# Kernel tuning notes

Hardware: AMD Instinct MI355X
Metric: run time of the kernel (lower is better)

## Reference

```python
import jax, jax.numpy as jnp
import numpy as np

DROP_PROB = 0.1
BLOCK_SIZE = 7  # odd -> no even-size trim branch
N, C, H, W = 64, 256, 28, 28


def conv3x3(x, w):
    # x: [N,C,H,W], w: [O,I,3,3], stride 1, SAME padding
    return jax.lax.conv_general_dilated(
        x, w, window_strides=(1, 1), padding='SAME',
        dimension_numbers=('NCHW', 'OIHW', 'NCHW'))


def setup_inputs() -> dict:
    key = jax.random.key(0)
    k1, k2, k3, k4 = jax.random.split(key, 4)
    x = jax.random.normal(k1, (N, C, H, W), jnp.float32)
    # learned conv weights for the two branches (layer3 and premodel.layer3)
    w_layer3 = jax.random.normal(k2, (C, C, 3, 3), jnp.float32) * 0.05
    w_pre = jax.random.normal(k3, (C, C, 3, 3), jnp.float32) * 0.05
    # uniform draws used for the Bernoulli(gamma) drop mask, shape (N,H,W)
    mask_u = jax.random.uniform(k4, (N, H, W), jnp.float32)
    return {'x': x, 'w_layer3': w_layer3, 'w_pre': w_pre, 'mask_u': mask_u}


def reference(x, w_layer3, w_pre, mask_u):
    gamma = DROP_PROB / (BLOCK_SIZE ** 2)
    a = conv3x3(x, w_layer3)   # x = self.layer3(x)
    b = conv3x3(x, w_pre)      # output4 = self.premodel.layer3(x)
    # mask = (rand(N,H,W) < gamma).float()
    mask = (mask_u < gamma).astype(x.dtype)  # [N,H,W]
    # block_mask = 1 - max_pool2d(mask, k=block_size, stride=1, pad=block_size//2)
    pooled = jax.lax.reduce_window(
        mask, -jnp.inf, jax.lax.max,
        window_dimensions=(1, BLOCK_SIZE, BLOCK_SIZE),
        window_strides=(1, 1, 1), padding='SAME')
    block_mask = 1.0 - pooled  # [N,H,W]
    # fused blend: keep layer3 output where block_mask==1, else premodel output
    out = jnp.where(block_mask[:, None, :, :] == 1.0, a, b)  # [N,C,H,W]
    # out * block_mask.numel() / block_mask.sum()
    scale = jnp.asarray(block_mask.size, x.dtype) / jnp.sum(block_mask)
    return out * scale
```

## Files before the change

### kernel.cpp

```cpp
#include <hip/hip_runtime.h>
#include <hip/hip_bf16.h>


typedef __bf16  bf16x8 __attribute__((ext_vector_type(8)));
typedef float   f32x4  __attribute__((ext_vector_type(4)));
typedef short   short8 __attribute__((ext_vector_type(8)));
typedef unsigned int u32;
typedef unsigned short u16;

#define XT_OFF     65536
#define WT_OFF     29556736
#define LISTA_OFF  31916032
#define LISTB_OFF  32116736
#define SLOT       22528

__device__ __forceinline__ u16 f2bf(float v) {
    u32 u = __float_as_uint(v);
    u32 r = (u + 0x7FFFu + ((u >> 16) & 1u)) >> 16;
    return (u16)r;
}

__device__ __forceinline__ void gll16(const void* g, void* l) {
    __builtin_amdgcn_global_load_lds(
        (const __attribute__((address_space(1))) u32*)g,
        (__attribute__((address_space(3))) u32*)l, 16, 0, 0);
}

__global__ void prep_kernel(const float* __restrict__ x,
                            const float* __restrict__ wl,
                            const float* __restrict__ wp,
                            const float* __restrict__ mu,
                            u16* __restrict__ xt, u16* __restrict__ wt,
                            int* __restrict__ listA, int* __restrict__ listB,
                            int* __restrict__ cntB, int* __restrict__ cntA) {
    int b = blockIdx.x, tid = threadIdx.x;
    if (b < 1920) {
        int n = b / 30, oh = b % 30;
        u16* row = xt + (size_t)(n * 30 + oh) * 30 * 256;
        if (oh == 0 || oh == 29) {
            u32* r32 = (u32*)row;
            #pragma unroll
            for (int i = 0; i < 15; ++i) r32[i * 256 + tid] = 0;
            return;
        }
        int h = oh - 1;
        row[tid] = 0;
        row[29 * 256 + tid] = 0;
        const float* src = x + ((size_t)(n * 256 + tid) * 28 + h) * 28;
        float f[28];
        #pragma unroll
        for (int q = 0; q < 7; ++q) {
            float4 v = *(const float4*)(src + q * 4);
            f[q * 4 + 0] = v.x; f[q * 4 + 1] = v.y;
            f[q * 4 + 2] = v.z; f[q * 4 + 3] = v.w;
        }
        #pragma unroll
        for (int w = 0; w < 28; ++w)
            row[(1 + w) * 256 + tid] = f2bf(f[w]);
    } else if (b < 2496) {
        int gid = (b - 1920) * 256 + tid;
        int base = gid << 3;
        int bb = base >> 12;
        int e = base & 4095;
        int t = bb >> 2, nq = bb & 3;
        int kk = t >> 3;
        int row = e >> 5, ps = (e & 31) >> 3;
        int c0 = (t & 7) * 32 + ((ps ^ ((row >> 1) & 3)) << 3);
        int o = nq * 128 + row;
        const float* wsrc = (o < 256) ? wl : wp;
        const float* wr = wsrc + ((size_t)(o & 255) * 256 + c0) * 9 + kk;
        short8 v;
        #pragma unroll
        for (int j = 0; j < 8; ++j) v[j] = (short)f2bf(wr[j * 9]);
        *(short8*)(wt + base) = v;
    } else {
        __shared__ int wbase[8];
        int m = (b - 2496) * 256 + tid;
        int n = m / 784, rem = m % 784;
        int h = rem / 28, w = rem % 28;
        const float g = (float)(0.1 / 49.0);
        const float* un = mu + n * 784;
        int p = 0;
        for (int dy = -3; dy <= 3; ++dy) {
            int hh = h + dy;
            if (hh < 0 || hh >= 28) continue;
            for (int dx = -3; dx <= 3; ++dx) {
                int ww = w + dx;
                if (ww < 0 || ww >= 28) continue;
                p |= (un[hh * 28 + ww] < g) ? 1 : 0;
            }
        }
        unsigned long long ball = __ballot(p);
        int wid = tid >> 6, ln = tid & 63;
        int c1 = __popcll(ball);
        if (ln == 0) {
            wbase[wid]     = atomicAdd(cntB, c1);
            wbase[4 + wid] = atomicAdd(cntA, 64 - c1);
        }
        __syncthreads();
        int rank1 = __popcll(ball & ((1ULL << ln) - 1));
        int rank0 = ln - rank1;
        if (p) listB[wbase[wid] + rank1] = m;
        else   listA[wbase[4 + wid] + rank0] = m;
    }
}

__global__ __launch_bounds__(256, 2)
void conv_kernel(const char* __restrict__ xt,
                 const char* __restrict__ wt,
                 const int* __restrict__ listA,
                 const int* __restrict__ listB,
                 const int* __restrict__ dropped,
                 float* __restrict__ out) {
    __shared__ char smem[55296];
    const int tid = threadIdx.x;
    const int lb = (blockIdx.x & 7) * 57 + (blockIdx.x >> 3);
    const int vt = lb >> 1;
    const int nh = lb & 1;
    const int cB = *dropped;
    const int cA = 50176 - cB;
    const int naT = (cA + 223) / 224;
    const int nbT = (cB + 223) / 224;
    if (vt >= naT + nbT) return;
    const int branch = (vt >= naT) ? 1 : 0;
    const int tix = branch ? (vt - naT) : vt;
    const int cnt = branch ? cB : cA;
    const int* lst = branch ? listB : listA;
    const int nq = branch * 2 + nh;
    const int lane = tid & 63, wave = tid >> 6;
    const int lane15 = lane & 15, grp = lane >> 4;
    const int wm = wave >> 1, wn = wave & 1;

    long pbA[4];
    {
        int swz = ((tid & 3) ^ ((tid >> 3) & 3)) << 4;
        #pragma unroll
        for (int i = 0; i < 4; ++i) {
            int r = i * 64 + (tid >> 2);
            int idx = tix * 224 + r;
            if (idx >= cnt) idx = cnt - 1;
            int m = lst[idx];
            int n = m / 784, rem = m % 784;
            pbA[i] = (long)(((n * 30 + rem / 28 + 1) * 30 + (rem % 28 + 1)) * 512
                            + swz);
        }
    }

    f32x4 acc[7][4];
    #pragma unroll
    for (int i = 0; i < 7; ++i)
        #pragma unroll
        for (int j = 0; j < 4; ++j)
            acc[i][j] = (f32x4){0.f, 0.f, 0.f, 0.f};

    const int so  = (grp ^ ((lane15 >> 1) & 3)) << 4;
    const int arb = wm * 7168 + (lane15 << 6) + so;
    const int brb = 14336 + wn * 4096 + (lane15 << 6) + so;

#define AON(TC) ((long)((TC) >> 3) / 3 * 15360 + (long)(((TC) >> 3) % 3) * 512 \
                 - 15872 + (long)(((TC) & 7) << 6))
#define STG(TC, SL) { char* sd_ = smem + (SL) * SLOT;                       \
        const long ao_ = AON(TC);                                           \
        gll16(xt + pbA[0] + ao_, sd_ + (tid << 4));                         \
        gll16(xt + pbA[1] + ao_, sd_ + 4096 + (tid << 4));                  \
        gll16(xt + pbA[2] + ao_, sd_ + 8192 + (tid << 4));                  \
        if (tid < 128) gll16(xt + pbA[3] + ao_, sd_ + 12288 + (tid << 4));  \
        const char* wb_ = wt + ((size_t)((TC) * 4 + nq) << 13);             \
        gll16(wb_ + (tid << 4), sd_ + 14336 + (tid << 4));                  \
        gll16(wb_ + 4096 + (tid << 4), sd_ + 18432 + (tid << 4)); }
#define DS_AV0(dst, SL) { const char* sb_ = smem + (SL) * SLOT;             \
        _Pragma("unroll")                                                   \
        for (int fm = 0; fm < 4; ++fm)                                      \
            dst[fm] = *(const bf16x8*)(sb_ + arb + (fm << 10)); }
#define DS_AV1(dst, SL) { const char* sb_ = smem + (SL) * SLOT + 4096;      \
        _Pragma("unroll")                                                   \
        for (int fm = 0; fm < 3; ++fm)                                      \
            dst[fm] = *(const bf16x8*)(sb_ + arb + (fm << 10)); }
#define DS_BV(dst, SL) { const char* sb_ = smem + (SL) * SLOT;              \
        _Pragma("unroll")                                                   \
        for (int fn = 0; fn < 4; ++fn)                                      \
            dst[fn] = *(const bf16x8*)(sb_ + brb + (fn << 10)); }
#define MM(A0_, NF, AV, BV) { __builtin_amdgcn_s_setprio(1);                \
        _Pragma("unroll")                                                   \
        for (int fm = 0; fm < (NF); ++fm)                                   \
            _Pragma("unroll")                                               \
            for (int fn = 0; fn < 4; ++fn)                                  \
                acc[(A0_)+fm][fn] = __builtin_amdgcn_mfma_f32_16x16x32_bf16( \
                    AV[fm], BV[fn], acc[(A0_)+fm][fn], 0, 0, 0);            \
        __builtin_amdgcn_s_setprio(0); }
#define LGKM(N) { asm volatile("s_waitcnt lgkmcnt(" #N ")" ::: "memory");   \
                  __builtin_amdgcn_sched_barrier(0); }
#define VM0     { asm volatile("s_waitcnt vmcnt(0)" ::: "memory");          \
                  __builtin_amdgcn_sched_barrier(0); }
#define BAR     asm volatile("s_barrier" ::: "memory")

    bf16x8 av0[4], av1[3], bv[4];

    STG(0, 0);
    VM0;
    BAR;

    for (int t = 0; t < 72; ++t) {
        const int sc = t & 1, ss = sc ^ 1;
        if (t < 71) STG(t + 1, ss);
        DS_AV0(av0, sc);
        DS_BV(bv, sc);
        DS_AV1(av1, sc);
        LGKM(3);
        MM(0, 4, av0, bv);
        LGKM(0);
        MM(4, 3, av1, bv);
        VM0;
        BAR;
    }

    float scale = 50176.0f / (float)(50176 - cB);
    float* ep = (float*)smem + wave * 2080;
    __syncthreads();
    #pragma unroll
    for (int rr = 0; rr < 4; ++rr) {
        const int r2 = rr & 1;
        const int mh = rr >> 1;
        const int nf = mh ? 3 : 4;
        for (int fm2 = 0; fm2 < nf; ++fm2)
            #pragma unroll
            for (int f2 = 0; f2 < 2; ++f2)
                #pragma unroll
                for (int j = 0; j < 4; ++j)
                    ep[(f2 * 16 + lane15) * 65 + fm2 * 16 + grp * 4 + j] =
                        acc[mh * 4 + fm2][r2 * 2 + f2][j];
        __syncthreads();
        {
            int gidx = tix * 224 + wm * 112 + mh * 64 + lane;
            if ((mh == 0 || lane < 48) && gidx < cnt) {
                int m = lst[gidx];
                int n = m / 784, rem = m % 784;
                size_t ob = (size_t)n * 200704 + rem;
                #pragma unroll
                for (int ch = 0; ch < 32; ++ch) {
                    int c = nh * 128 + wn * 64 + r2 * 32 + ch;
                    out[ob + (size_t)c * 784] = ep[ch * 65 + lane] * scale;
                }
            }
        }
        __syncthreads();
    }
#undef AON
#undef STG
#undef DS_AV0
#undef DS_AV1
#undef DS_BV
#undef MM
#undef LGKM
#undef VM0
#undef BAR
}

extern "C" void kernel_launch(void* const* d_in, const int* in_sizes, int n_in,
                              void* d_out, int out_size, void* d_ws, size_t ws_size,
                              hipStream_t stream) {
    const float* x  = (const float*)d_in[0];
    const float* wl = (const float*)d_in[1];
    const float* wp = (const float*)d_in[2];
    const float* mu = (const float*)d_in[3];
    float* out = (float*)d_out;
    char* ws = (char*)d_ws;

    int* cntB = (int*)ws;
    int* cntA = (int*)(ws + 4);
    u16* xt = (u16*)(ws + XT_OFF);
    u16* wt = (u16*)(ws + WT_OFF);
    int* listA = (int*)(ws + LISTA_OFF);
    int* listB = (int*)(ws + LISTB_OFF);

    hipMemsetAsync(ws, 0, 8, stream);

    prep_kernel<<<2692, 256, 0, stream>>>(x, wl, wp, mu, xt, wt,
                                          listA, listB, cntB, cntA);
    conv_kernel<<<456, 256, 0, stream>>>((const char*)xt, (const char*)wt,
                                         listA, listB, cntB, out);
}
```

Baseline: 116.0 us.

## Split prep into coalesced LDS-transpose kernel and per-image mask list builder

The NCHW-to-padded-NHWC bf16 conversion moves into its own kernel. That kernel reads contiguous float4 chunks per image and channel quarter, stages them in LDS, and writes channel-pair packed u32 values, replacing the old strided per-thread row reads and 2-byte scattered writes. The drop-mask list build now runs one block per image: it caches the uniforms in LDS, scans them with a block-level prefix, and issues one atomic per list per block instead of one per wave. The cost is an extra kernel launch, plus a serial prefix loop and heavy LDS use in the transpose kernel.

```diff
diff --git a/kernel.cpp b/kernel.cpp
--- a/kernel.cpp
+++ b/kernel.cpp
@@ -26,39 +26,65 @@
         (__attribute__((address_space(3))) u32*)l, 16, 0, 0);
 }
 
-__global__ void prep_kernel(const float* __restrict__ x,
-                            const float* __restrict__ wl,
-                            const float* __restrict__ wp,
-                            const float* __restrict__ mu,
-                            u16* __restrict__ xt, u16* __restrict__ wt,
-                            int* __restrict__ listA, int* __restrict__ listB,
-                            int* __restrict__ cntB, int* __restrict__ cntA) {
+__global__ __launch_bounds__(256)
+void prep_xt(const float* __restrict__ x, u16* __restrict__ xt) {
+    __shared__ u16 sm[64 * 790];
+    const int n = blockIdx.x >> 2, ct = blockIdx.x & 3;
+    const int tid = threadIdx.x;
+    u32* b32 = (u32*)(xt + (size_t)n * 230400);
+
+    if (ct == 0) {
+        #pragma unroll
+        for (int i = 0; i < 15; ++i) {
+            int k = i * 256 + tid;
+            b32[k] = 0;
+            b32[111360 + k] = 0;
+        }
+        #pragma unroll
+        for (int i = 0; i < 14; ++i) {
+            int k = i * 256 + tid;
+            int oh = 1 + (k >> 7), c2 = k & 127;
+            b32[(oh * 30) * 128 + c2] = 0;
+            b32[(oh * 30 + 29) * 128 + c2] = 0;
+        }
+    }
+
+    const float4* s4 = (const float4*)(x + (size_t)n * 200704) + ct * 12544;
+    char* smb = (char*)sm;
+    #pragma unroll 7
+    for (int i = 0; i < 49; ++i) {
+        int q = i * 256 + tid;
+        float4 v = s4[q];
+        int lc = q / 196, r = q % 196;
+        u32* dst = (u32*)(smb + lc * 1580 + r * 8);
+        dst[0] = (u32)f2bf(v.x) | ((u32)f2bf(v.y) << 16);
+        dst[1] = (u32)f2bf(v.z) | ((u32)f2bf(v.w) << 16);
+    }
+    __syncthreads();
+
+    const int cpp = tid & 31, sl = tid >> 5;
+    const char* srow0 = smb + (2 * cpp) * 1580;
+    const char* srow1 = srow0 + 1580;
+    #pragma unroll 7
+    for (int t2 = 0; t2 < 98; ++t2) {
+        int hw = sl * 98 + t2;
+        int h = hw / 28, w = hw % 28;
+        u32 v = (u32)*(const u16*)(srow0 + hw * 2)
+              | ((u32)*(const u16*)(srow1 + hw * 2) << 16);
+        b32[((1 + h) * 30 + 1 + w) * 128 + ct * 32 + cpp] = v;
+    }
+}
+
+__global__ __launch_bounds__(256)
+void prep_rest(const float* __restrict__ wl,
+               const float* __restrict__ wp,
+               const float* __restrict__ mu,
+               u16* __restrict__ wt,
+               int* __restrict__ listA, int* __restrict__ listB,
+               int* __restrict__ cntB, int* __restrict__ cntA) {
     int b = blockIdx.x, tid = threadIdx.x;
-    if (b < 1920) {
-        int n = b / 30, oh = b % 30;
-        u16* row = xt + (size_t)(n * 30 + oh) * 30 * 256;
-        if (oh == 0 || oh == 29) {
-            u32* r32 = (u32*)row;
-            #pragma unroll
-            for (int i = 0; i < 15; ++i) r32[i * 256 + tid] = 0;
-            return;
-        }
-        int h = oh - 1;
-        row[tid] = 0;
-        row[29 * 256 + tid] = 0;
-        const float* src = x + ((size_t)(n * 256 + tid) * 28 + h) * 28;
-        float f[28];
-        #pragma unroll
-        for (int q = 0; q < 7; ++q) {
-            float4 v = *(const float4*)(src + q * 4);
-            f[q * 4 + 0] = v.x; f[q * 4 + 1] = v.y;
-            f[q * 4 + 2] = v.z; f[q * 4 + 3] = v.w;
-        }
-        #pragma unroll
-        for (int w = 0; w < 28; ++w)
-            row[(1 + w) * 256 + tid] = f2bf(f[w]);
-    } else if (b < 2496) {
-        int gid = (b - 1920) * 256 + tid;
+    if (b < 576) {
+        int gid = b * 256 + tid;
         int base = gid << 3;
         int bb = base >> 12;
         int e = base & 4095;
@@ -74,34 +100,66 @@
         for (int j = 0; j < 8; ++j) v[j] = (short)f2bf(wr[j * 9]);
         *(short8*)(wt + base) = v;
     } else {
-        __shared__ int wbase[8];
-        int m = (b - 2496) * 256 + tid;
-        int n = m / 784, rem = m % 784;
-        int h = rem / 28, w = rem % 28;
+        __shared__ float uf[784];
+        __shared__ int cnts[2][16];
+        __shared__ int bases[2];
+        const int n = b - 576;
+        const float* un = mu + n * 784;
+        for (int i = tid; i < 784; i += 256) uf[i] = un[i];
+        __syncthreads();
         const float g = (float)(0.1 / 49.0);
-        const float* un = mu + n * 784;
-        int p = 0;
-        for (int dy = -3; dy <= 3; ++dy) {
-            int hh = h + dy;
-            if (hh < 0 || hh >= 28) continue;
-            for (int dx = -3; dx <= 3; ++dx) {
-                int ww = w + dx;
-                if (ww < 0 || ww >= 28) continue;
-                p |= (un[hh * 28 + ww] < g) ? 1 : 0;
+        const int wid = tid >> 6, ln = tid & 63;
+        unsigned long long balB[4], balA[4];
+        int pbit[4];
+        #pragma unroll
+        for (int it = 0; it < 4; ++it) {
+            int i = it * 256 + tid;
+            int a = (i < 784);
+            int p = 0;
+            if (a) {
+                int h = i / 28, w = i % 28;
+                for (int dy = -3; dy <= 3; ++dy) {
+                    int hh = h + dy;
+                    if (hh < 0 || hh >= 28) continue;
+                    for (int dx = -3; dx <= 3; ++dx) {
+                        int ww = w + dx;
+                        if (ww < 0 || ww >= 28) continue;
+                        p |= (uf[hh * 28 + ww] < g) ? 1 : 0;
+                    }
+                }
             }
-        }
-        unsigned long long ball = __ballot(p);
-        int wid = tid >> 6, ln = tid & 63;
-        int c1 = __popcll(ball);
-        if (ln == 0) {
-            wbase[wid]     = atomicAdd(cntB, c1);
-            wbase[4 + wid] = atomicAdd(cntA, 64 - c1);
-        }
-        __syncthreads();
-        int rank1 = __popcll(ball & ((1ULL << ln) - 1));
-        int rank0 = ln - rank1;
-        if (p) listB[wbase[wid] + rank1] = m;
-        else   listA[wbase[4 + wid] + rank0] = m;
+            pbit[it] = p;
+            balB[it] = __ballot(a && p);
+            balA[it] = __ballot(a != 0);
+            if (ln == 0) {
+                int c1 = __popcll(balB[it]);
+                cnts[1][it * 4 + wid] = c1;
+                cnts[0][it * 4 + wid] = __popcll(balA[it]) - c1;
+            }
+        }
+        __syncthreads();
+        if (tid == 0) {
+            int tB = 0, tA = 0;
+            #pragma unroll
+            for (int s = 0; s < 16; ++s) { tB += cnts[1][s]; tA += cnts[0][s]; }
+            bases[1] = atomicAdd(cntB, tB);
+            bases[0] = atomicAdd(cntA, tA);
+        }
+        __syncthreads();
+        #pragma unroll
+        for (int it = 0; it < 4; ++it) {
+            int i = it * 256 + tid;
+            if (i >= 784) continue;
+            int slot = it * 4 + wid;
+            int offB = 0, offA = 0;
+            for (int s = 0; s < slot; ++s) { offB += cnts[1][s]; offA += cnts[0][s]; }
+            unsigned long long below = (1ULL << ln) - 1;
+            int r1 = __popcll(balB[it] & below);
+            int rA = __popcll(balA[it] & below) - r1;
+            int m = n * 784 + i;
+            if (pbit[it]) listB[bases[1] + offB + r1] = m;
+            else          listA[bases[0] + offA + rA] = m;
+        }
     }
 }
 
@@ -275,8 +333,8 @@
 
     hipMemsetAsync(ws, 0, 8, stream);
 
-    prep_kernel<<<2692, 256, 0, stream>>>(x, wl, wp, mu, xt, wt,
-                                          listA, listB, cntB, cntA);
+    prep_xt<<<256, 256, 0, stream>>>(x, xt);
+    prep_rest<<<640, 256, 0, stream>>>(wl, wp, mu, wt, listA, listB, cntB, cntA);
     conv_kernel<<<456, 256, 0, stream>>>((const char*)xt, (const char*)wt,
                                          listA, listB, cntB, out);
 }
```

New measurement: 104.8 us. 9.6% less time.
